# Performance work log

Hardware: AMD Instinct MI355X
Metric: run time of the kernel (lower is better)

Reference implementation:

```python
import jax, jax.numpy as jnp
import numpy as np


def setup_inputs() -> dict:
    key = jax.random.key(0)
    kq, kk, kv = jax.random.split(key, 3)
    B, N, M, H, D = 4, 2048, 2048, 8, 64
    queries = jax.random.normal(kq, (B, N, H, D), dtype=jnp.float32)
    keys = jax.random.normal(kk, (B, M, H, D), dtype=jnp.float32)
    values = jax.random.normal(kv, (B, M, H, D), dtype=jnp.float32)
    return {"queries": queries, "keys": keys, "values": values}


def reference(queries, keys, values):
    # queries: [B,N,H,D], keys/values: [B,M,H,D]
    D = queries.shape[3]
    softmax_temp = 1.0 / (D ** 0.5)
    QK = jnp.einsum('bnhd,bmhd->bnmh', queries, keys)  # [B,N,M,H]
    A = jax.nn.softmax(softmax_temp * QK, axis=2)      # softmax over M
    queried_values = jnp.einsum('bnmh,bmhd->bnhd', A, values)
    attention_weight = jnp.transpose(A, (0, 3, 1, 2))  # [B,H,N,M]
    return (queried_values, attention_weight)
```

## Files before the change

kernel.cpp:

```cpp
#include <hip/hip_runtime.h>

typedef __bf16 bf16x8 __attribute__((ext_vector_type(8)));
typedef float floatx4 __attribute__((ext_vector_type(4)));
typedef unsigned short ushort8 __attribute__((ext_vector_type(8)));
typedef unsigned short ushort4v __attribute__((ext_vector_type(4)));

#define MFMA(a, b, c) __builtin_amdgcn_mfma_f32_16x16x32_bf16((a), (b), (c), 0, 0, 0)

__device__ __forceinline__ unsigned short f2bf(float x) {
  union { float f; unsigned u; } v; v.f = x;
  unsigned r = v.u + 0x7FFFu + ((v.u >> 16) & 1u);
  return (unsigned short)(r >> 16);
}

__global__ __launch_bounds__(256)
void prep(const float* __restrict__ K, const float* __restrict__ V,
          unsigned short* __restrict__ Kb, unsigned short* __restrict__ Vt)
{
  int id = blockIdx.x * 256 + threadIdx.x;
  int isV = id >> 19;
  int cch = id & 524287;
  int bh = cch >> 14;
  int mt = (cch >> 9) & 31;
  int g  = cch & 511;
  int r  = g >> 3;
  int s  = g & 7;
  int e8 = s ^ (r & 7);
  int b = bh >> 3, h = bh & 7;
  ushort8 o;
  if (!isV) {
    const float* p = K + (((size_t)(b * 2048 + mt * 64 + r) * 8 + h) * 64 + e8 * 8);
    float4 x0 = *(const float4*)p;
    float4 x1 = *(const float4*)(p + 4);
    o[0] = f2bf(x0.x); o[1] = f2bf(x0.y); o[2] = f2bf(x0.z); o[3] = f2bf(x0.w);
    o[4] = f2bf(x1.x); o[5] = f2bf(x1.y); o[6] = f2bf(x1.z); o[7] = f2bf(x1.w);
    *(ushort8*)(Kb + (size_t)cch * 8) = o;
  } else {
    const float* p = V + (((size_t)(b * 2048 + mt * 64 + e8 * 8) * 8 + h) * 64 + r);
    #pragma unroll
    for (int j = 0; j < 8; ++j) o[j] = f2bf(p[(size_t)j * 512]);
    *(ushort8*)(Vt + (size_t)cch * 8) = o;
  }
}

__device__ __forceinline__ void stage1k(const unsigned short* gsrc, unsigned short* lds,
                                        int w, int l)
{
  const char* g = (const char*)gsrc + w * 1024 + l * 16;
  char* sd = (char*)lds + w * 1024;
  __builtin_amdgcn_global_load_lds((const __attribute__((address_space(1))) unsigned int*)g,
                                   (__attribute__((address_space(3))) unsigned int*)sd, 16, 0, 0);
}

__device__ __forceinline__ bf16x8 frag(const unsigned short* lds, int r, int bo)
{
  int slot = ((bo >> 4) ^ r) & 7;
  return *(const bf16x8*)((const char*)lds + r * 128 + (slot << 4));
}

__global__ __launch_bounds__(512, 4)
void attn_fwd(const float* __restrict__ Q, const unsigned short* __restrict__ Kb,
              const unsigned short* __restrict__ Vt,
              float* __restrict__ outQV, float* __restrict__ outA)
{
  __shared__ __align__(16) unsigned short Ks[3][4096];
  __shared__ __align__(16) unsigned short Vs[3][4096];
  __shared__ __align__(16) unsigned short As[8192];

  const int tid = threadIdx.x;
  const int w  = tid >> 6;
  const int l  = tid & 63;
  const int c  = l & 15;
  const int q4 = l >> 4;

  const int bx = (blockIdx.x & 7) * 64 + (blockIdx.x >> 3);
  const int qt = bx & 15;
  const int bh = bx >> 4;
  const int h  = bh & 7;
  const int b  = bh >> 3;
  const int q0 = qt * 128;

  const float scale = 0.125f * 1.44269504088896340736f;

  const size_t base = (size_t)b * (2048 * 512) + (size_t)h * 64;
  const float* Qb = Q + base + (size_t)q0 * 512;

  const unsigned short* Kt0 = Kb + (size_t)bh * (32 * 4096);
  const unsigned short* Vt0 = Vt + (size_t)bh * (32 * 4096);

  bf16x8 bQ0, bQ1;
  {
    const float* qp = Qb + (size_t)(16 * w + c) * 512 + q4 * 8;
    float4 qa0 = *(const float4*)(qp);
    float4 qa1 = *(const float4*)(qp + 4);
    float4 qb0 = *(const float4*)(qp + 32);
    float4 qb1 = *(const float4*)(qp + 36);
    ushort8 t0, t1;
    t0[0]=f2bf(qa0.x*scale); t0[1]=f2bf(qa0.y*scale); t0[2]=f2bf(qa0.z*scale); t0[3]=f2bf(qa0.w*scale);
    t0[4]=f2bf(qa1.x*scale); t0[5]=f2bf(qa1.y*scale); t0[6]=f2bf(qa1.z*scale); t0[7]=f2bf(qa1.w*scale);
    t1[0]=f2bf(qb0.x*scale); t1[1]=f2bf(qb0.y*scale); t1[2]=f2bf(qb0.z*scale); t1[3]=f2bf(qb0.w*scale);
    t1[4]=f2bf(qb1.x*scale); t1[5]=f2bf(qb1.y*scale); t1[6]=f2bf(qb1.z*scale); t1[7]=f2bf(qb1.w*scale);
    bQ0 = __builtin_bit_cast(bf16x8, t0);
    bQ1 = __builtin_bit_cast(bf16x8, t1);
  }

  stage1k(Kt0, Ks[0], w, l);
  stage1k(Kt0 + 4096, Ks[1], w, l);
  asm volatile("s_waitcnt vmcnt(1)" ::: "memory");
  __builtin_amdgcn_s_barrier();
  __builtin_amdgcn_sched_barrier(0);

  float lsum[4] = {0.f, 0.f, 0.f, 0.f};
  int cur = 0;
  for (int mt = 0; mt < 32; ++mt) {
    int nx = (mt + 2 < 32) ? mt + 2 : 31;
    int sb = cur + 2; if (sb >= 3) sb -= 3;
    stage1k(Kt0 + (size_t)nx * 4096, Ks[sb], w, l);
    __builtin_amdgcn_sched_barrier(0);
    const unsigned short* Kc = Ks[cur];
    __builtin_amdgcn_s_setprio(1);
    #pragma unroll
    for (int t = 0; t < 4; ++t) {
      bf16x8 aK0 = frag(Kc, t * 16 + c, q4 * 16);
      bf16x8 aK1 = frag(Kc, t * 16 + c, 64 + q4 * 16);
      floatx4 acc = {0.f, 0.f, 0.f, 0.f};
      acc = MFMA(aK0, bQ0, acc);
      acc = MFMA(aK1, bQ1, acc);
      #pragma unroll
      for (int i = 0; i < 4; ++i) lsum[i] += __builtin_amdgcn_exp2f(acc[i]);
    }
    __builtin_amdgcn_s_setprio(0);
    __builtin_amdgcn_sched_barrier(0);
    asm volatile("s_waitcnt vmcnt(1)" ::: "memory");
    __builtin_amdgcn_s_barrier();
    __builtin_amdgcn_sched_barrier(0);
    cur = cur + 1; if (cur >= 3) cur -= 3;
  }
  float rs = (lsum[0] + lsum[1]) + (lsum[2] + lsum[3]);
  rs += __shfl_xor(rs, 16);
  rs += __shfl_xor(rs, 32);
  const float rcp = 1.0f / rs;

  floatx4 Oacc[4];
  #pragma unroll
  for (int t = 0; t < 4; ++t) Oacc[t] = (floatx4){0.f, 0.f, 0.f, 0.f};

  const int arow = 16 * w + c;
  float* aRowP = outA + (((size_t)bh * 2048 + q0 + arow) * 2048) + q4 * 4;

  asm volatile("s_waitcnt vmcnt(0)" ::: "memory");
  stage1k(Kt0, Ks[0], w, l);
  stage1k(Vt0, Vs[0], w, l);
  stage1k(Kt0 + 4096, Ks[1], w, l);
  stage1k(Vt0 + 4096, Vs[1], w, l);
  asm volatile("s_waitcnt vmcnt(2)" ::: "memory");
  __builtin_amdgcn_s_barrier();
  __builtin_amdgcn_sched_barrier(0);

  cur = 0;
  for (int mt = 0; mt < 32; ++mt) {
    int nx = (mt + 2 < 32) ? mt + 2 : 31;
    int sb = cur + 2; if (sb >= 3) sb -= 3;
    stage1k(Kt0 + (size_t)nx * 4096, Ks[sb], w, l);
    stage1k(Vt0 + (size_t)nx * 4096, Vs[sb], w, l);
    __builtin_amdgcn_sched_barrier(0);
    const unsigned short* Kc = Ks[cur];
    const unsigned short* Vc = Vs[cur];
    const int mc = mt * 64;
    __builtin_amdgcn_s_setprio(1);
    #pragma unroll
    for (int t = 0; t < 4; ++t) {
      bf16x8 aK0 = frag(Kc, t * 16 + c, q4 * 16);
      bf16x8 aK1 = frag(Kc, t * 16 + c, 64 + q4 * 16);
      floatx4 acc = {0.f, 0.f, 0.f, 0.f};
      acc = MFMA(aK0, bQ0, acc);
      acc = MFMA(aK1, bQ1, acc);
      floatx4 av;
      av[0] = __builtin_amdgcn_exp2f(acc[0]) * rcp;
      av[1] = __builtin_amdgcn_exp2f(acc[1]) * rcp;
      av[2] = __builtin_amdgcn_exp2f(acc[2]) * rcp;
      av[3] = __builtin_amdgcn_exp2f(acc[3]) * rcp;
      *(floatx4*)(aRowP + mc + t * 16) = av;
      ushort4v us = { f2bf(av[0]), f2bf(av[1]), f2bf(av[2]), f2bf(av[3]) };
      int bo = t * 32 + q4 * 8;
      int slot = ((bo >> 4) ^ arow) & 7;
      *(ushort4v*)((char*)As + arow * 128 + (slot << 4) + (bo & 15)) = us;
    }
    {
      int s0 = ((q4) ^ arow) & 7;
      int s1 = ((4 + q4) ^ arow) & 7;
      bf16x8 aP0 = *(const bf16x8*)((const char*)As + arow * 128 + (s0 << 4));
      bf16x8 aP1 = *(const bf16x8*)((const char*)As + arow * 128 + (s1 << 4));
      #pragma unroll
      for (int t = 0; t < 4; ++t) {
        bf16x8 bV0 = frag(Vc, t * 16 + c, q4 * 16);
        bf16x8 bV1 = frag(Vc, t * 16 + c, 64 + q4 * 16);
        Oacc[t] = MFMA(aP0, bV0, Oacc[t]);
        Oacc[t] = MFMA(aP1, bV1, Oacc[t]);
      }
    }
    __builtin_amdgcn_s_setprio(0);
    __builtin_amdgcn_sched_barrier(0);
    asm volatile("s_waitcnt vmcnt(6)" ::: "memory");
    __builtin_amdgcn_s_barrier();
    __builtin_amdgcn_sched_barrier(0);
    cur = cur + 1; if (cur >= 3) cur -= 3;
  }

  #pragma unroll
  for (int t = 0; t < 4; ++t) {
    #pragma unroll
    for (int i = 0; i < 4; ++i) {
      outQV[base + (size_t)(q0 + 16 * w + q4 * 4 + i) * 512 + t * 16 + c] = Oacc[t][i];
    }
  }
}

extern "C" void kernel_launch(void* const* d_in, const int* in_sizes, int n_in,
                              void* d_out, int out_size, void* d_ws, size_t ws_size,
                              hipStream_t stream)
{
  const float* Q = (const float*)d_in[0];
  const float* K = (const float*)d_in[1];
  const float* V = (const float*)d_in[2];
  float* outQV = (float*)d_out;
  float* outA  = (float*)d_out + 4194304;

  unsigned short* Kb = (unsigned short*)d_ws;
  unsigned short* Vt = (unsigned short*)d_ws + 4194304;

  prep<<<dim3(4096), dim3(256), 0, stream>>>(K, V, Kb, Vt);
  attn_fwd<<<dim3(512), dim3(512), 0, stream>>>(Q, Kb, Vt, outQV, outA);
}
```

Before: 636.1 us.

## Coalesce V transpose via LDS in prep and double-buffer two K/V tiles per stage

The prep kernel now has each block handle one 64-row tile and transposes V through shared memory, so the old strided scalar V reads become coalesced float4 loads. The attention kernel replaces its triple-buffered one-tile pipeline with a double-buffered pipeline that loads two 64-key tiles per stage. That halves the number of barriers and waitcnts per pass and amortizes sync cost. The trade-off is more LDS per block and waits that are stricter (vmcnt(0) in the first pass), which could expose load latency.

```diff
diff --git a/kernel.cpp b/kernel.cpp
--- a/kernel.cpp
+++ b/kernel.cpp
@@ -17,29 +17,55 @@
 void prep(const float* __restrict__ K, const float* __restrict__ V,
           unsigned short* __restrict__ Kb, unsigned short* __restrict__ Vt)
 {
-  int id = blockIdx.x * 256 + threadIdx.x;
-  int isV = id >> 19;
-  int cch = id & 524287;
-  int bh = cch >> 14;
-  int mt = (cch >> 9) & 31;
-  int g  = cch & 511;
-  int r  = g >> 3;
-  int s  = g & 7;
-  int e8 = s ^ (r & 7);
-  int b = bh >> 3, h = bh & 7;
-  ushort8 o;
-  if (!isV) {
-    const float* p = K + (((size_t)(b * 2048 + mt * 64 + r) * 8 + h) * 64 + e8 * 8);
-    float4 x0 = *(const float4*)p;
-    float4 x1 = *(const float4*)(p + 4);
-    o[0] = f2bf(x0.x); o[1] = f2bf(x0.y); o[2] = f2bf(x0.z); o[3] = f2bf(x0.w);
-    o[4] = f2bf(x1.x); o[5] = f2bf(x1.y); o[6] = f2bf(x1.z); o[7] = f2bf(x1.w);
-    *(ushort8*)(Kb + (size_t)cch * 8) = o;
-  } else {
-    const float* p = V + (((size_t)(b * 2048 + mt * 64 + e8 * 8) * 8 + h) * 64 + r);
-    #pragma unroll
-    for (int j = 0; j < 8; ++j) o[j] = f2bf(p[(size_t)j * 512]);
-    *(ushort8*)(Vt + (size_t)cch * 8) = o;
+  __shared__ float Vl[64 * 68];
+
+  const int bx = blockIdx.x;
+  const int mt = bx & 31;
+  const int bh = bx >> 5;
+  const int b  = bh >> 3, h = bh & 7;
+  const int tid = threadIdx.x;
+  const int r  = tid >> 2;
+  const int cq = tid & 3;
+
+  const size_t inbase = ((size_t)(b * 2048 + mt * 64 + r) * 8 + h) * 64 + cq * 16;
+  unsigned short* ktile = Kb + ((size_t)bh * 32 + mt) * 4096;
+  unsigned short* vtile = Vt + ((size_t)bh * 32 + mt) * 4096;
+
+  {
+    float4 a0 = *(const float4*)(K + inbase);
+    float4 a1 = *(const float4*)(K + inbase + 4);
+    float4 a2 = *(const float4*)(K + inbase + 8);
+    float4 a3 = *(const float4*)(K + inbase + 12);
+    ushort8 o0 = { f2bf(a0.x), f2bf(a0.y), f2bf(a0.z), f2bf(a0.w),
+                   f2bf(a1.x), f2bf(a1.y), f2bf(a1.z), f2bf(a1.w) };
+    ushort8 o1 = { f2bf(a2.x), f2bf(a2.y), f2bf(a2.z), f2bf(a2.w),
+                   f2bf(a3.x), f2bf(a3.y), f2bf(a3.z), f2bf(a3.w) };
+    *(ushort8*)(ktile + r * 64 + (((cq * 2)     ^ (r & 7)) * 8)) = o0;
+    *(ushort8*)(ktile + r * 64 + (((cq * 2 + 1) ^ (r & 7)) * 8)) = o1;
+  }
+
+  {
+    float4 a0 = *(const float4*)(V + inbase);
+    float4 a1 = *(const float4*)(V + inbase + 4);
+    float4 a2 = *(const float4*)(V + inbase + 8);
+    float4 a3 = *(const float4*)(V + inbase + 12);
+    float vv[16] = { a0.x,a0.y,a0.z,a0.w, a1.x,a1.y,a1.z,a1.w,
+                     a2.x,a2.y,a2.z,a2.w, a3.x,a3.y,a3.z,a3.w };
+    #pragma unroll
+    for (int j = 0; j < 16; ++j) Vl[(cq * 16 + j) * 68 + r] = vv[j];
+  }
+  __syncthreads();
+  {
+    float4 w0 = *(const float4*)&Vl[r * 68 + cq * 16];
+    float4 w1 = *(const float4*)&Vl[r * 68 + cq * 16 + 4];
+    float4 w2 = *(const float4*)&Vl[r * 68 + cq * 16 + 8];
+    float4 w3 = *(const float4*)&Vl[r * 68 + cq * 16 + 12];
+    ushort8 p0 = { f2bf(w0.x), f2bf(w0.y), f2bf(w0.z), f2bf(w0.w),
+                   f2bf(w1.x), f2bf(w1.y), f2bf(w1.z), f2bf(w1.w) };
+    ushort8 p1 = { f2bf(w2.x), f2bf(w2.y), f2bf(w2.z), f2bf(w2.w),
+                   f2bf(w3.x), f2bf(w3.y), f2bf(w3.z), f2bf(w3.w) };
+    *(ushort8*)(vtile + r * 64 + (((cq * 2)     ^ (r & 7)) * 8)) = p0;
+    *(ushort8*)(vtile + r * 64 + (((cq * 2 + 1) ^ (r & 7)) * 8)) = p1;
   }
 }
 
@@ -63,9 +89,10 @@
               const unsigned short* __restrict__ Vt,
               float* __restrict__ outQV, float* __restrict__ outA)
 {
-  __shared__ __align__(16) unsigned short Ks[3][4096];
-  __shared__ __align__(16) unsigned short Vs[3][4096];
-  __shared__ __align__(16) unsigned short As[8192];
+  __shared__ __align__(16) unsigned short pool[40960];
+  unsigned short* Kp = pool;
+  unsigned short* Vp = pool + 16384;
+  unsigned short* As = pool + 32768;
 
   const int tid = threadIdx.x;
   const int w  = tid >> 6;
@@ -104,37 +131,40 @@
     bQ1 = __builtin_bit_cast(bf16x8, t1);
   }
 
-  stage1k(Kt0, Ks[0], w, l);
-  stage1k(Kt0 + 4096, Ks[1], w, l);
-  asm volatile("s_waitcnt vmcnt(1)" ::: "memory");
+  stage1k(Kt0,        Kp,        w, l);
+  stage1k(Kt0 + 4096, Kp + 4096, w, l);
+  asm volatile("s_waitcnt vmcnt(0)" ::: "memory");
   __builtin_amdgcn_s_barrier();
   __builtin_amdgcn_sched_barrier(0);
 
   float lsum[4] = {0.f, 0.f, 0.f, 0.f};
-  int cur = 0;
-  for (int mt = 0; mt < 32; ++mt) {
-    int nx = (mt + 2 < 32) ? mt + 2 : 31;
-    int sb = cur + 2; if (sb >= 3) sb -= 3;
-    stage1k(Kt0 + (size_t)nx * 4096, Ks[sb], w, l);
-    __builtin_amdgcn_sched_barrier(0);
-    const unsigned short* Kc = Ks[cur];
+  for (int s = 0; s < 16; ++s) {
+    const int pp = s & 1;
+    if (s < 15) {
+      stage1k(Kt0 + (size_t)(2 * s + 2) * 4096, Kp + (pp ^ 1) * 8192,        w, l);
+      stage1k(Kt0 + (size_t)(2 * s + 3) * 4096, Kp + (pp ^ 1) * 8192 + 4096, w, l);
+    }
+    __builtin_amdgcn_sched_barrier(0);
     __builtin_amdgcn_s_setprio(1);
     #pragma unroll
-    for (int t = 0; t < 4; ++t) {
-      bf16x8 aK0 = frag(Kc, t * 16 + c, q4 * 16);
-      bf16x8 aK1 = frag(Kc, t * 16 + c, 64 + q4 * 16);
-      floatx4 acc = {0.f, 0.f, 0.f, 0.f};
-      acc = MFMA(aK0, bQ0, acc);
-      acc = MFMA(aK1, bQ1, acc);
+    for (int j = 0; j < 2; ++j) {
+      const unsigned short* Kc = Kp + (pp * 2 + j) * 4096;
       #pragma unroll
-      for (int i = 0; i < 4; ++i) lsum[i] += __builtin_amdgcn_exp2f(acc[i]);
+      for (int t = 0; t < 4; ++t) {
+        bf16x8 aK0 = frag(Kc, t * 16 + c, q4 * 16);
+        bf16x8 aK1 = frag(Kc, t * 16 + c, 64 + q4 * 16);
+        floatx4 acc = {0.f, 0.f, 0.f, 0.f};
+        acc = MFMA(aK0, bQ0, acc);
+        acc = MFMA(aK1, bQ1, acc);
+        #pragma unroll
+        for (int i = 0; i < 4; ++i) lsum[i] += __builtin_amdgcn_exp2f(acc[i]);
+      }
     }
     __builtin_amdgcn_s_setprio(0);
     __builtin_amdgcn_sched_barrier(0);
-    asm volatile("s_waitcnt vmcnt(1)" ::: "memory");
+    asm volatile("s_waitcnt vmcnt(0)" ::: "memory");
     __builtin_amdgcn_s_barrier();
     __builtin_amdgcn_sched_barrier(0);
-    cur = cur + 1; if (cur >= 3) cur -= 3;
   }
   float rs = (lsum[0] + lsum[1]) + (lsum[2] + lsum[3]);
   rs += __shfl_xor(rs, 16);
@@ -148,63 +178,66 @@
   const int arow = 16 * w + c;
   float* aRowP = outA + (((size_t)bh * 2048 + q0 + arow) * 2048) + q4 * 4;
 
+  stage1k(Kt0,        Kp,        w, l);
+  stage1k(Kt0 + 4096, Kp + 4096, w, l);
+  stage1k(Vt0,        Vp,        w, l);
+  stage1k(Vt0 + 4096, Vp + 4096, w, l);
   asm volatile("s_waitcnt vmcnt(0)" ::: "memory");
-  stage1k(Kt0, Ks[0], w, l);
-  stage1k(Vt0, Vs[0], w, l);
-  stage1k(Kt0 + 4096, Ks[1], w, l);
-  stage1k(Vt0 + 4096, Vs[1], w, l);
-  asm volatile("s_waitcnt vmcnt(2)" ::: "memory");
   __builtin_amdgcn_s_barrier();
   __builtin_amdgcn_sched_barrier(0);
 
-  cur = 0;
-  for (int mt = 0; mt < 32; ++mt) {
-    int nx = (mt + 2 < 32) ? mt + 2 : 31;
-    int sb = cur + 2; if (sb >= 3) sb -= 3;
-    stage1k(Kt0 + (size_t)nx * 4096, Ks[sb], w, l);
-    stage1k(Vt0 + (size_t)nx * 4096, Vs[sb], w, l);
-    __builtin_amdgcn_sched_barrier(0);
-    const unsigned short* Kc = Ks[cur];
-    const unsigned short* Vc = Vs[cur];
-    const int mc = mt * 64;
+  for (int s = 0; s < 16; ++s) {
+    const int pp = s & 1;
+    if (s < 15) {
+      stage1k(Kt0 + (size_t)(2 * s + 2) * 4096, Kp + (pp ^ 1) * 8192,        w, l);
+      stage1k(Kt0 + (size_t)(2 * s + 3) * 4096, Kp + (pp ^ 1) * 8192 + 4096, w, l);
+      stage1k(Vt0 + (size_t)(2 * s + 2) * 4096, Vp + (pp ^ 1) * 8192,        w, l);
+      stage1k(Vt0 + (size_t)(2 * s + 3) * 4096, Vp + (pp ^ 1) * 8192 + 4096, w, l);
+    }
+    __builtin_amdgcn_sched_barrier(0);
     __builtin_amdgcn_s_setprio(1);
     #pragma unroll
-    for (int t = 0; t < 4; ++t) {
-      bf16x8 aK0 = frag(Kc, t * 16 + c, q4 * 16);
-      bf16x8 aK1 = frag(Kc, t * 16 + c, 64 + q4 * 16);
-      floatx4 acc = {0.f, 0.f, 0.f, 0.f};
-      acc = MFMA(aK0, bQ0, acc);
-      acc = MFMA(aK1, bQ1, acc);
-      floatx4 av;
-      av[0] = __builtin_amdgcn_exp2f(acc[0]) * rcp;
-      av[1] = __builtin_amdgcn_exp2f(acc[1]) * rcp;
-      av[2] = __builtin_amdgcn_exp2f(acc[2]) * rcp;
-      av[3] = __builtin_amdgcn_exp2f(acc[3]) * rcp;
-      *(floatx4*)(aRowP + mc + t * 16) = av;
-      ushort4v us = { f2bf(av[0]), f2bf(av[1]), f2bf(av[2]), f2bf(av[3]) };
-      int bo = t * 32 + q4 * 8;
-      int slot = ((bo >> 4) ^ arow) & 7;
-      *(ushort4v*)((char*)As + arow * 128 + (slot << 4) + (bo & 15)) = us;
-    }
-    {
-      int s0 = ((q4) ^ arow) & 7;
-      int s1 = ((4 + q4) ^ arow) & 7;
-      bf16x8 aP0 = *(const bf16x8*)((const char*)As + arow * 128 + (s0 << 4));
-      bf16x8 aP1 = *(const bf16x8*)((const char*)As + arow * 128 + (s1 << 4));
+    for (int j = 0; j < 2; ++j) {
+      const unsigned short* Kc = Kp + (pp * 2 + j) * 4096;
+      const unsigned short* Vc = Vp + (pp * 2 + j) * 4096;
+      const int mc = (2 * s + j) * 64;
       #pragma unroll
       for (int t = 0; t < 4; ++t) {
-        bf16x8 bV0 = frag(Vc, t * 16 + c, q4 * 16);
-        bf16x8 bV1 = frag(Vc, t * 16 + c, 64 + q4 * 16);
-        Oacc[t] = MFMA(aP0, bV0, Oacc[t]);
-        Oacc[t] = MFMA(aP1, bV1, Oacc[t]);
+        bf16x8 aK0 = frag(Kc, t * 16 + c, q4 * 16);
+        bf16x8 aK1 = frag(Kc, t * 16 + c, 64 + q4 * 16);
+        floatx4 acc = {0.f, 0.f, 0.f, 0.f};
+        acc = MFMA(aK0, bQ0, acc);
+        acc = MFMA(aK1, bQ1, acc);
+        floatx4 av;
+        av[0] = __builtin_amdgcn_exp2f(acc[0]) * rcp;
+        av[1] = __builtin_amdgcn_exp2f(acc[1]) * rcp;
+        av[2] = __builtin_amdgcn_exp2f(acc[2]) * rcp;
+        av[3] = __builtin_amdgcn_exp2f(acc[3]) * rcp;
+        *(floatx4*)(aRowP + mc + t * 16) = av;
+        ushort4v us = { f2bf(av[0]), f2bf(av[1]), f2bf(av[2]), f2bf(av[3]) };
+        int bo = t * 32 + q4 * 8;
+        int slot = ((bo >> 4) ^ arow) & 7;
+        *(ushort4v*)((char*)As + arow * 128 + (slot << 4) + (bo & 15)) = us;
       }
+      {
+        int s0 = ((q4) ^ arow) & 7;
+        int s1 = ((4 + q4) ^ arow) & 7;
+        bf16x8 aP0 = *(const bf16x8*)((const char*)As + arow * 128 + (s0 << 4));
+        bf16x8 aP1 = *(const bf16x8*)((const char*)As + arow * 128 + (s1 << 4));
+        #pragma unroll
+        for (int t = 0; t < 4; ++t) {
+          bf16x8 bV0 = frag(Vc, t * 16 + c, q4 * 16);
+          bf16x8 bV1 = frag(Vc, t * 16 + c, 64 + q4 * 16);
+          Oacc[t] = MFMA(aP0, bV0, Oacc[t]);
+          Oacc[t] = MFMA(aP1, bV1, Oacc[t]);
+        }
+      }
     }
     __builtin_amdgcn_s_setprio(0);
     __builtin_amdgcn_sched_barrier(0);
-    asm volatile("s_waitcnt vmcnt(6)" ::: "memory");
+    asm volatile("s_waitcnt vmcnt(8)" ::: "memory");
     __builtin_amdgcn_s_barrier();
     __builtin_amdgcn_sched_barrier(0);
-    cur = cur + 1; if (cur >= 3) cur -= 3;
   }
 
   #pragma unroll
@@ -229,6 +262,6 @@
   unsigned short* Kb = (unsigned short*)d_ws;
   unsigned short* Vt = (unsigned short*)d_ws + 4194304;
 
-  prep<<<dim3(4096), dim3(256), 0, stream>>>(K, V, Kb, Vt);
+  prep<<<dim3(1024), dim3(256), 0, stream>>>(K, V, Kb, Vt);
   attn_fwd<<<dim3(512), dim3(512), 0, stream>>>(Q, Kb, Vt, outQV, outA);
 }
```

Result: no change. 627.3 us (-1.4%).
